# Kernel tuning notes

Hardware: AMD Instinct MI355X
Metric: run time of the kernel (lower is better)

## Reference

```python
import jax, jax.numpy as jnp
import numpy as np

N = 50000          # num nodes
E = 800000         # num edges (avg degree 16)
C_IN = 64          # input channels
TOWERS = 4
F_IN = C_IN // TOWERS       # 16 (divide_input=True)
OUT = 128
F_OUT = OUT // TOWERS       # 32
NUM_AGG = 4                 # mean, std, max, min
NUM_SC = 3                  # identity, amplification, attenuation
AVG_LOG_DEG = float(np.log(17.0))  # deg histogram: all nodes degree 16 -> log(16+1)


def setup_inputs() -> dict:
    key = jax.random.key(0)
    ks = jax.random.split(key, 10)
    nodes = jax.random.normal(ks[0], (N, C_IN), dtype=jnp.float32)
    senders = jax.random.randint(ks[1], (E,), 0, N)
    receivers = jax.random.randint(ks[2], (E,), 0, N)
    # per-tower pre-MLP: Linear(2*F_IN -> F_IN), pre_layers=1 (no activation)
    pre_w = jax.random.normal(ks[3], (TOWERS, 2 * F_IN, F_IN), dtype=jnp.float32) / np.sqrt(2 * F_IN)
    pre_b = jnp.zeros((TOWERS, F_IN), dtype=jnp.float32)
    # per-tower post-MLP: Linear(F_IN + F_IN*12 -> F_OUT), post_layers=1
    post_in = F_IN + F_IN * NUM_AGG * NUM_SC  # 208
    post_w = jax.random.normal(ks[4], (TOWERS, post_in, F_OUT), dtype=jnp.float32) / np.sqrt(post_in)
    post_b = jnp.zeros((TOWERS, F_OUT), dtype=jnp.float32)
    # final linear: TOWERS*F_OUT -> OUT
    lin_w = jax.random.normal(ks[5], (TOWERS * F_OUT, OUT), dtype=jnp.float32) / np.sqrt(TOWERS * F_OUT)
    lin_b = jnp.zeros((OUT,), dtype=jnp.float32)
    return {"nodes": nodes, "senders": senders, "receivers": receivers,
            "pre_w": pre_w, "pre_b": pre_b, "post_w": post_w, "post_b": post_b,
            "lin_w": lin_w, "lin_b": lin_b}


def reference(nodes, senders, receivers, pre_w, pre_b, post_w, post_b, lin_w, lin_b):
    # divide_input=True: split channels across towers -> [N, T, F_IN]
    x = nodes.reshape(N, TOWERS, F_IN)
    x_i = x[senders]                                  # [E, T, F_IN]
    x_j = x[receivers]                                # [E, T, F_IN]
    h = jnp.concatenate([x_i, x_j], axis=-1)          # [E, T, 2*F_IN]
    # per-tower pre-MLP (single linear), vectorized over towers
    msg = jnp.einsum('etf,tfo->eto', h, pre_w) + pre_b  # [E, T, F_IN]

    # degree-scaled multi-aggregator segment reduce over receivers
    count = jax.ops.segment_sum(jnp.ones((E,), dtype=msg.dtype), receivers, num_segments=N)  # [N]
    d = jnp.clip(count, 1.0, None)
    inv_d = (1.0 / d)[:, None, None]
    mean = jax.ops.segment_sum(msg, receivers, num_segments=N) * inv_d           # [N,T,F]
    mean_sq = jax.ops.segment_sum(msg * msg, receivers, num_segments=N) * inv_d
    std = jnp.sqrt(jax.nn.relu(mean_sq - mean * mean) + 1e-5)
    has_nb = (count > 0)[:, None, None]
    mx = jax.ops.segment_max(msg, receivers, num_segments=N)
    mx = jnp.where(has_nb, mx, 0.0)
    mn = -jax.ops.segment_max(-msg, receivers, num_segments=N)
    mn = jnp.where(has_nb, mn, 0.0)
    agg = jnp.concatenate([mean, std, mx, mn], axis=-1)  # [N, T, 4*F_IN]

    # scalers: identity, amplification, attenuation (degree clamped to >= 1)
    log_d = jnp.log(d + 1.0)[:, None, None]
    amp = log_d / AVG_LOG_DEG
    att = AVG_LOG_DEG / log_d
    scaled = jnp.concatenate([agg, agg * amp, agg * att], axis=-1)  # [N, T, 12*F_IN]

    out = jnp.concatenate([x, scaled], axis=-1)                     # [N, T, 13*F_IN]
    outs = jnp.einsum('ntf,tfo->nto', out, post_w) + post_b         # [N, T, F_OUT]
    flat = outs.reshape(N, TOWERS * F_OUT)                          # [N, 128]
    return flat @ lin_w + lin_b                                     # [N, OUT]
```

## Files before the change

### kernel.cpp

```cpp
#include <hip/hip_runtime.h>

#define AVG_LOG_DEG 2.8332133440562162f
#define CAP 64

typedef __attribute__((ext_vector_type(8))) short short8;
typedef __attribute__((ext_vector_type(4))) float f32x4;

static __device__ __forceinline__ float bl(unsigned u) { return __uint_as_float(u << 16); }
static __device__ __forceinline__ float bh(unsigned u) { return __uint_as_float(u & 0xffff0000u); }
static __device__ __forceinline__ unsigned short f2b(float f) {
    unsigned u = __float_as_uint(f);
    return (unsigned short)((u + 0x7fffu + ((u >> 16) & 1u)) >> 16);
}
static __device__ __forceinline__ unsigned pk(unsigned short lo, unsigned short hi) {
    return (unsigned)lo | ((unsigned)hi << 16);
}


__global__ void k_init(int* __restrict__ cursor, int n) {
    int i = blockIdx.x * 256 + threadIdx.x;
    if (i < n) cursor[i] = 0;
}

__global__ __launch_bounds__(256) void k_scatter2(
    const int* __restrict__ send, const int* __restrict__ recv,
    int* __restrict__ cursor, int* __restrict__ slots,
    int e, int nps)
{
    int slice = blockIdx.x & 7;
    int chunk = blockIdx.x >> 3;
    int base = chunk * 2048;
    int lo = slice * nps;
    #pragma unroll
    for (int it = 0; it < 8; ++it) {
        int i = base + it * 256 + threadIdx.x;
        if (i < e) {
            int r = recv[i];
            if ((unsigned)(r - lo) < (unsigned)nps) {
                int p = atomicAdd(&cursor[r], 1);
                if (p < CAP) slots[(size_t)r * CAP + p] = send[i];
            }
        }
    }
}


__global__ void k_prew(const float* __restrict__ post_w, const float* __restrict__ lin_w,
                       unsigned short* __restrict__ postT, unsigned short* __restrict__ linT) {
    int i = blockIdx.x * 256 + threadIdx.x;
    if (i < 28672) {
        int t = i / (32 * 224);
        int r = i % (32 * 224);
        int nn = r / 224;
        int k = r % 224;
        float wv;
        if (k < 192)      wv = post_w[((size_t)t * 208 + 16 + k) * 32 + nn];
        else if (k < 208) wv = post_w[((size_t)t * 208 + (k - 192)) * 32 + nn];
        else              wv = 0.f;
        postT[i] = f2b(wv);
    }
    int j = i - 28672;
    if (j >= 0 && j < 16384) {
        int nn = j >> 7, k = j & 127;
        linT[j] = f2b(lin_w[k * 128 + nn]);
    }
}


__global__ __launch_bounds__(256) void k_pre(
    const float* __restrict__ nodes,
    const float* __restrict__ pre_w,
    float* __restrict__ Y, int n)
{
    int lane = threadIdx.x & 63;
    int node = blockIdx.x * 4 + (threadIdx.x >> 6);
    if (node >= n) return;
    int t = lane >> 4, f = lane & 15;
    float w[16];
    #pragma unroll
    for (int k = 0; k < 16; ++k)
        w[k] = pre_w[(t * 32 + k) * 16 + f];
    const float4* xp = reinterpret_cast<const float4*>(nodes + (size_t)node * 64 + t * 16);
    float4 x0 = xp[0], x1 = xp[1], x2 = xp[2], x3 = xp[3];
    float xs[16] = {x0.x, x0.y, x0.z, x0.w, x1.x, x1.y, x1.z, x1.w,
                    x2.x, x2.y, x2.z, x2.w, x3.x, x3.y, x3.z, x3.w};
    float y = 0.f;
    #pragma unroll
    for (int k = 0; k < 16; ++k)
        y = fmaf(xs[k], w[k], y);
    Y[(size_t)node * 64 + lane] = y;
}


__global__ __launch_bounds__(256) void k_agg(
    const float* __restrict__ nodes,
    const float* __restrict__ pre_w,
    const float* __restrict__ pre_b,
    const int* __restrict__ cursor,
    const int* __restrict__ slots, const float* __restrict__ Y,
    unsigned short* __restrict__ aggh, int n)
{
    int lane = threadIdx.x & 63;
    int node = blockIdx.x * 4 + (threadIdx.x >> 6);
    if (node >= n) return;
    int t = lane >> 4, f = lane & 15;

    float w[16];
    #pragma unroll
    for (int k = 0; k < 16; ++k)
        w[k] = pre_w[(t * 32 + 16 + k) * 16 + f];
    const float4* xp = reinterpret_cast<const float4*>(nodes + (size_t)node * 64 + t * 16);
    float4 x0 = xp[0], x1 = xp[1], x2 = xp[2], x3 = xp[3];
    float xs[16] = {x0.x, x0.y, x0.z, x0.w, x1.x, x1.y, x1.z, x1.w,
                    x2.x, x2.y, x2.z, x2.w, x3.x, x3.y, x3.z, x3.w};
    float hjw = pre_b[t * 16 + f];
    #pragma unroll
    for (int k = 0; k < 16; ++k)
        hjw = fmaf(xs[k], w[k], hjw);

    int d = min(cursor[node], CAP);
    const int* sl = slots + (size_t)node * CAP;
    const float* Yp = Y + lane;
    float s = 0.f, s2 = 0.f, mx = -INFINITY, mn = INFINITY;
    int e = 0;
    for (; e + 4 <= d; e += 4) {
        int i0 = sl[e], i1 = sl[e + 1], i2 = sl[e + 2], i3 = sl[e + 3];
        float m0 = Yp[(size_t)i0 * 64] + hjw;
        float m1 = Yp[(size_t)i1 * 64] + hjw;
        float m2 = Yp[(size_t)i2 * 64] + hjw;
        float m3 = Yp[(size_t)i3 * 64] + hjw;
        s += (m0 + m1) + (m2 + m3);
        s2 = fmaf(m0, m0, s2); s2 = fmaf(m1, m1, s2);
        s2 = fmaf(m2, m2, s2); s2 = fmaf(m3, m3, s2);
        mx = fmaxf(mx, fmaxf(fmaxf(m0, m1), fmaxf(m2, m3)));
        mn = fminf(mn, fminf(fminf(m0, m1), fminf(m2, m3)));
    }
    for (; e < d; ++e) {
        int i0 = sl[e];
        float m0 = Yp[(size_t)i0 * 64] + hjw;
        s += m0;
        s2 = fmaf(m0, m0, s2);
        mx = fmaxf(mx, m0);
        mn = fminf(mn, m0);
    }

    float dc = fmaxf((float)d, 1.f);
    float inv = 1.f / dc;
    float mean = s * inv;
    float var = fmaf(-mean, mean, s2 * inv);
    float sd = sqrtf(fmaxf(var, 0.f) + 1e-5f);
    if (d == 0) { mx = 0.f; mn = 0.f; }

    unsigned short* ag = aggh + (size_t)node * 256 + t * 64 + f;
    ag[0]  = f2b(mean);
    ag[16] = f2b(sd);
    ag[32] = f2b(mx);
    ag[48] = f2b(mn);
}


__global__ __launch_bounds__(256) void k_post(
    const float* __restrict__ nodes,
    const unsigned short* __restrict__ aggh,
    const int* __restrict__ deg,
    const unsigned short* __restrict__ postT,
    const unsigned short* __restrict__ linT,
    const float* __restrict__ post_b,
    const float* __restrict__ lin_b,
    float* __restrict__ out, int n)
{
    __shared__ unsigned short sV[32 * 256];
    __shared__ unsigned short sFlat[32 * 128];
    __shared__ float sAmp[32], sAtt[32];

    int tid = threadIdx.x;
    int n0 = blockIdx.x * 32;

    if (tid < 32) {
        int g = min(n0 + tid, n - 1);
        float dc = fmaxf((float)min(deg[g], CAP), 1.f);
        float ld = logf(dc + 1.f);
        sAmp[tid] = ld * (1.f / AVG_LOG_DEG);
        sAtt[tid] = AVG_LOG_DEG / ld;
    }
    __syncthreads();

    int w = tid >> 6, lane = tid & 63;
    int quad = lane >> 4, mr = lane & 15;
    int mstrip = w & 1, nhalf = w >> 1;
    int nn = tid >> 3, j8 = tid & 7;
    int sw = nn & 7;
    int gn = min(n0 + nn, n - 1);
    int rsw = mr & 7;

    for (int t = 0; t < 4; ++t) {
        short8 bfr[7];
        {
            const unsigned short* bp = postT + (size_t)(t * 32 + nhalf * 16 + mr) * 224 + quad * 8;
            #pragma unroll
            for (int kk = 0; kk < 7; ++kk)
                bfr[kk] = *reinterpret_cast<const short8*>(bp + kk * 32);
        }

        {
            float amp = sAmp[nn], att = sAtt[nn];
            unsigned short* row = &sV[nn * 256];
            uint4 a = *reinterpret_cast<const uint4*>(aggh + (size_t)gn * 256 + t * 64 + j8 * 8);
            *reinterpret_cast<uint4*>(row + (j8 ^ sw) * 8) = a;
            unsigned uu[4] = {a.x, a.y, a.z, a.w};
            unsigned short pa[8], pb[8];
            #pragma unroll
            for (int q = 0; q < 4; ++q) {
                float lo = bl(uu[q]), hi = bh(uu[q]);
                pa[2*q]   = f2b(lo * amp); pa[2*q+1] = f2b(hi * amp);
                pb[2*q]   = f2b(lo * att); pb[2*q+1] = f2b(hi * att);
            }
            uint4 wa, wb;
            wa.x = pk(pa[0], pa[1]); wa.y = pk(pa[2], pa[3]);
            wa.z = pk(pa[4], pa[5]); wa.w = pk(pa[6], pa[7]);
            wb.x = pk(pb[0], pb[1]); wb.y = pk(pb[2], pb[3]);
            wb.z = pk(pb[4], pb[5]); wb.w = pk(pb[6], pb[7]);
            *reinterpret_cast<uint4*>(row + (8  + (j8 ^ sw)) * 8) = wa;
            *reinterpret_cast<uint4*>(row + (16 + (j8 ^ sw)) * 8) = wb;
            uint4 xw; xw.x = 0; xw.y = 0; xw.z = 0; xw.w = 0;
            if (j8 < 2) {
                const float4* xp = reinterpret_cast<const float4*>(nodes + (size_t)gn * 64 + t * 16 + j8 * 8);
                float4 xa = xp[0], xb = xp[1];
                xw.x = pk(f2b(xa.x), f2b(xa.y)); xw.y = pk(f2b(xa.z), f2b(xa.w));
                xw.z = pk(f2b(xb.x), f2b(xb.y)); xw.w = pk(f2b(xb.z), f2b(xb.w));
            }
            *reinterpret_cast<uint4*>(row + (24 + (j8 ^ sw)) * 8) = xw;
        }
        __syncthreads();

        f32x4 acc = {0.f, 0.f, 0.f, 0.f};
        const unsigned short* av0 = &sV[(mstrip * 16 + mr) * 256];
        #pragma unroll
        for (int kk = 0; kk < 7; ++kk) {
            int c = kk * 4 + quad;
            int pc = (c & ~7) | ((c & 7) ^ rsw);
            short8 avv = *reinterpret_cast<const short8*>(av0 + pc * 8);
            acc = __builtin_amdgcn_mfma_f32_16x16x32_bf16(avv, bfr[kk], acc, 0, 0, 0);
        }

        int col = t * 32 + nhalf * 16 + mr;
        float pbv = post_b[col];
        int cc = col >> 3, co = col & 7;
        #pragma unroll
        for (int i = 0; i < 4; ++i) {
            int rowf = mstrip * 16 + quad * 4 + i;
            int pc = (cc & ~7) | ((cc & 7) ^ (rowf & 7));
            sFlat[rowf * 128 + pc * 8 + co] = f2b(acc[i] + pbv);
        }
        __syncthreads();
    }

    f32x4 facc[4];
    #pragma unroll
    for (int nt = 0; nt < 4; ++nt) { facc[nt].x = 0.f; facc[nt].y = 0.f; facc[nt].z = 0.f; facc[nt].w = 0.f; }

    const unsigned short* af0 = &sFlat[(mstrip * 16 + mr) * 128];
    #pragma unroll
    for (int kk = 0; kk < 4; ++kk) {
        int c = kk * 4 + quad;
        int pc = (c & ~7) | ((c & 7) ^ rsw);
        short8 avv = *reinterpret_cast<const short8*>(af0 + pc * 8);
        #pragma unroll
        for (int nt = 0; nt < 4; ++nt) {
            short8 bv = *reinterpret_cast<const short8*>(
                linT + (size_t)(nhalf * 64 + nt * 16 + mr) * 128 + kk * 32 + quad * 8);
            facc[nt] = __builtin_amdgcn_mfma_f32_16x16x32_bf16(avv, bv, facc[nt], 0, 0, 0);
        }
    }

    #pragma unroll
    for (int nt = 0; nt < 4; ++nt) {
        int col = nhalf * 64 + nt * 16 + mr;
        float lb = lin_b[col];
        #pragma unroll
        for (int i = 0; i < 4; ++i) {
            int node = n0 + mstrip * 16 + quad * 4 + i;
            if (node < n) out[(size_t)node * 128 + col] = facc[nt][i] + lb;
        }
    }
}

extern "C" void kernel_launch(void* const* d_in, const int* in_sizes, int n_in,
                              void* d_out, int out_size, void* d_ws, size_t ws_size,
                              hipStream_t stream)
{
    const float* nodes  = (const float*)d_in[0];
    const int*   send   = (const int*)d_in[1];
    const int*   recv   = (const int*)d_in[2];
    const float* pre_w  = (const float*)d_in[3];
    const float* pre_b  = (const float*)d_in[4];
    const float* post_w = (const float*)d_in[5];
    const float* post_b = (const float*)d_in[6];
    const float* lin_w  = (const float*)d_in[7];
    const float* lin_b  = (const float*)d_in[8];
    float* out = (float*)d_out;

    int N = in_sizes[0] / 64;
    int E = in_sizes[1];
    int Npad = (N + 255) & ~255;

    int* cursor = (int*)d_ws;
    int* slots  = cursor + Npad;
    float* Y    = (float*)(slots + (size_t)Npad * CAP);
    unsigned short* aggh  = (unsigned short*)(Y + (size_t)Npad * 64);
    unsigned short* postT = aggh + (size_t)Npad * 256;
    unsigned short* linT  = postT + 28672;

    int nbN = (N + 255) / 256;
    int nps = (N + 7) / 8;
    int nbS = 8 * ((E + 2047) / 2048);

    k_prew    <<<176, 256, 0, stream>>>(post_w, lin_w, postT, linT);
    k_init    <<<nbN, 256, 0, stream>>>(cursor, N);
    k_scatter2<<<nbS, 256, 0, stream>>>(send, recv, cursor, slots, E, nps);
    k_pre     <<<(N + 3) / 4, 256, 0, stream>>>(nodes, pre_w, Y, N);
    k_agg     <<<(N + 3) / 4, 256, 0, stream>>>(nodes, pre_w, pre_b, cursor, slots, Y, aggh, N);
    k_post    <<<(N + 31) / 32, 256, 0, stream>>>(nodes, aggh, cursor, postT, linT,
                                                  post_b, lin_b, out, N);
}
```

Measured before the change: 213.7 us.

## Merge setup kernels into one launch and aggregate two nodes per wavefront

Folds the weight-transpose, cursor-init and node pre-projection kernels into one launch split by block ranges, which removes two kernel launches and the gaps between them. The aggregation kernel now gives each half-wavefront of 32 lanes one node. Each lane handles two features through float2 gathers and an 8-way unrolled neighbour loop, and writes packed bf16 pairs. This targets more memory-level parallelism and fewer issued loads per gathered row, at the cost of more registers per lane and half the lanes per node.

```diff
diff --git a/kernel.cpp b/kernel.cpp
--- a/kernel.cpp
+++ b/kernel.cpp
@@ -17,10 +17,56 @@
 }
 
 
-__global__ void k_init(int* __restrict__ cursor, int n) {
-    int i = blockIdx.x * 256 + threadIdx.x;
-    if (i < n) cursor[i] = 0;
-}
+__global__ __launch_bounds__(256) void k_setup(
+    const float* __restrict__ nodes, const float* __restrict__ pre_w,
+    const float* __restrict__ post_w, const float* __restrict__ lin_w,
+    float* __restrict__ Y, unsigned short* __restrict__ postT,
+    unsigned short* __restrict__ linT, int* __restrict__ cursor,
+    int n, int A, int nbN)
+{
+    int b = blockIdx.x;
+    if (b < A) {
+        int lane = threadIdx.x & 63;
+        int node = b * 4 + (threadIdx.x >> 6);
+        if (node >= n) return;
+        int t = lane >> 4, f = lane & 15;
+        float w[16];
+        #pragma unroll
+        for (int k = 0; k < 16; ++k)
+            w[k] = pre_w[(t * 32 + k) * 16 + f];
+        const float4* xp = reinterpret_cast<const float4*>(nodes + (size_t)node * 64 + t * 16);
+        float4 x0 = xp[0], x1 = xp[1], x2 = xp[2], x3 = xp[3];
+        float xs[16] = {x0.x, x0.y, x0.z, x0.w, x1.x, x1.y, x1.z, x1.w,
+                        x2.x, x2.y, x2.z, x2.w, x3.x, x3.y, x3.z, x3.w};
+        float y = 0.f;
+        #pragma unroll
+        for (int k = 0; k < 16; ++k)
+            y = fmaf(xs[k], w[k], y);
+        Y[(size_t)node * 64 + lane] = y;
+    } else if (b < A + 176) {
+        int i = (b - A) * 256 + threadIdx.x;
+        if (i < 28672) {
+            int t = i / (32 * 224);
+            int r = i % (32 * 224);
+            int nn = r / 224;
+            int k = r % 224;
+            float wv;
+            if (k < 192)      wv = post_w[((size_t)t * 208 + 16 + k) * 32 + nn];
+            else if (k < 208) wv = post_w[((size_t)t * 208 + (k - 192)) * 32 + nn];
+            else              wv = 0.f;
+            postT[i] = f2b(wv);
+        }
+        int j = i - 28672;
+        if (j >= 0 && j < 16384) {
+            int nn = j >> 7, k = j & 127;
+            linT[j] = f2b(lin_w[k * 128 + nn]);
+        }
+    } else {
+        int i = (b - A - 176) * 256 + threadIdx.x;
+        if (i < n) cursor[i] = 0;
+    }
+}
+
 
 __global__ __launch_bounds__(256) void k_scatter2(
     const int* __restrict__ send, const int* __restrict__ recv,
@@ -45,53 +91,6 @@
 }
 
 
-__global__ void k_prew(const float* __restrict__ post_w, const float* __restrict__ lin_w,
-                       unsigned short* __restrict__ postT, unsigned short* __restrict__ linT) {
-    int i = blockIdx.x * 256 + threadIdx.x;
-    if (i < 28672) {
-        int t = i / (32 * 224);
-        int r = i % (32 * 224);
-        int nn = r / 224;
-        int k = r % 224;
-        float wv;
-        if (k < 192)      wv = post_w[((size_t)t * 208 + 16 + k) * 32 + nn];
-        else if (k < 208) wv = post_w[((size_t)t * 208 + (k - 192)) * 32 + nn];
-        else              wv = 0.f;
-        postT[i] = f2b(wv);
-    }
-    int j = i - 28672;
-    if (j >= 0 && j < 16384) {
-        int nn = j >> 7, k = j & 127;
-        linT[j] = f2b(lin_w[k * 128 + nn]);
-    }
-}
-
-
-__global__ __launch_bounds__(256) void k_pre(
-    const float* __restrict__ nodes,
-    const float* __restrict__ pre_w,
-    float* __restrict__ Y, int n)
-{
-    int lane = threadIdx.x & 63;
-    int node = blockIdx.x * 4 + (threadIdx.x >> 6);
-    if (node >= n) return;
-    int t = lane >> 4, f = lane & 15;
-    float w[16];
-    #pragma unroll
-    for (int k = 0; k < 16; ++k)
-        w[k] = pre_w[(t * 32 + k) * 16 + f];
-    const float4* xp = reinterpret_cast<const float4*>(nodes + (size_t)node * 64 + t * 16);
-    float4 x0 = xp[0], x1 = xp[1], x2 = xp[2], x3 = xp[3];
-    float xs[16] = {x0.x, x0.y, x0.z, x0.w, x1.x, x1.y, x1.z, x1.w,
-                    x2.x, x2.y, x2.z, x2.w, x3.x, x3.y, x3.z, x3.w};
-    float y = 0.f;
-    #pragma unroll
-    for (int k = 0; k < 16; ++k)
-        y = fmaf(xs[k], w[k], y);
-    Y[(size_t)node * 64 + lane] = y;
-}
-
-
 __global__ __launch_bounds__(256) void k_agg(
     const float* __restrict__ nodes,
     const float* __restrict__ pre_w,
@@ -101,61 +100,79 @@
     unsigned short* __restrict__ aggh, int n)
 {
     int lane = threadIdx.x & 63;
-    int node = blockIdx.x * 4 + (threadIdx.x >> 6);
+    int half = lane >> 5, sub = lane & 31;
+    int node = blockIdx.x * 8 + (threadIdx.x >> 6) * 2 + half;
     if (node >= n) return;
-    int t = lane >> 4, f = lane & 15;
-
-    float w[16];
-    #pragma unroll
-    for (int k = 0; k < 16; ++k)
-        w[k] = pre_w[(t * 32 + 16 + k) * 16 + f];
-    const float4* xp = reinterpret_cast<const float4*>(nodes + (size_t)node * 64 + t * 16);
-    float4 x0 = xp[0], x1 = xp[1], x2 = xp[2], x3 = xp[3];
-    float xs[16] = {x0.x, x0.y, x0.z, x0.w, x1.x, x1.y, x1.z, x1.w,
-                    x2.x, x2.y, x2.z, x2.w, x3.x, x3.y, x3.z, x3.w};
-    float hjw = pre_b[t * 16 + f];
-    #pragma unroll
-    for (int k = 0; k < 16; ++k)
-        hjw = fmaf(xs[k], w[k], hjw);
+    int t = sub >> 3;
+    int f0 = (sub & 7) * 2;
+
+    float2 hjw;
+    {
+        const float4* xp = reinterpret_cast<const float4*>(nodes + (size_t)node * 64 + t * 16);
+        float4 x0 = xp[0], x1 = xp[1], x2 = xp[2], x3 = xp[3];
+        float xs[16] = {x0.x, x0.y, x0.z, x0.w, x1.x, x1.y, x1.z, x1.w,
+                        x2.x, x2.y, x2.z, x2.w, x3.x, x3.y, x3.z, x3.w};
+        hjw.x = pre_b[t * 16 + f0];
+        hjw.y = pre_b[t * 16 + f0 + 1];
+        #pragma unroll
+        for (int k = 0; k < 16; ++k) {
+            hjw.x = fmaf(xs[k], pre_w[(t * 32 + 16 + k) * 16 + f0],     hjw.x);
+            hjw.y = fmaf(xs[k], pre_w[(t * 32 + 16 + k) * 16 + f0 + 1], hjw.y);
+        }
+    }
 
     int d = min(cursor[node], CAP);
     const int* sl = slots + (size_t)node * CAP;
-    const float* Yp = Y + lane;
-    float s = 0.f, s2 = 0.f, mx = -INFINITY, mn = INFINITY;
+    const float* Yp = Y + sub * 2;
+
+    float2 s = {0.f, 0.f}, s2 = {0.f, 0.f};
+    float2 mx = {-INFINITY, -INFINITY}, mn = {INFINITY, INFINITY};
+
     int e = 0;
-    for (; e + 4 <= d; e += 4) {
-        int i0 = sl[e], i1 = sl[e + 1], i2 = sl[e + 2], i3 = sl[e + 3];
-        float m0 = Yp[(size_t)i0 * 64] + hjw;
-        float m1 = Yp[(size_t)i1 * 64] + hjw;
-        float m2 = Yp[(size_t)i2 * 64] + hjw;
-        float m3 = Yp[(size_t)i3 * 64] + hjw;
-        s += (m0 + m1) + (m2 + m3);
-        s2 = fmaf(m0, m0, s2); s2 = fmaf(m1, m1, s2);
-        s2 = fmaf(m2, m2, s2); s2 = fmaf(m3, m3, s2);
-        mx = fmaxf(mx, fmaxf(fmaxf(m0, m1), fmaxf(m2, m3)));
-        mn = fminf(mn, fminf(fminf(m0, m1), fminf(m2, m3)));
+    for (; e + 8 <= d; e += 8) {
+        int idx[8];
+        #pragma unroll
+        for (int q = 0; q < 8; ++q) idx[q] = sl[e + q];
+        float2 v[8];
+        #pragma unroll
+        for (int q = 0; q < 8; ++q)
+            v[q] = *reinterpret_cast<const float2*>(Yp + (size_t)idx[q] * 64);
+        #pragma unroll
+        for (int q = 0; q < 8; ++q) {
+            float2 m;
+            m.x = v[q].x + hjw.x; m.y = v[q].y + hjw.y;
+            s.x += m.x; s.y += m.y;
+            s2.x = fmaf(m.x, m.x, s2.x); s2.y = fmaf(m.y, m.y, s2.y);
+            mx.x = fmaxf(mx.x, m.x); mx.y = fmaxf(mx.y, m.y);
+            mn.x = fminf(mn.x, m.x); mn.y = fminf(mn.y, m.y);
+        }
     }
     for (; e < d; ++e) {
         int i0 = sl[e];
-        float m0 = Yp[(size_t)i0 * 64] + hjw;
-        s += m0;
-        s2 = fmaf(m0, m0, s2);
-        mx = fmaxf(mx, m0);
-        mn = fminf(mn, m0);
+        float2 v = *reinterpret_cast<const float2*>(Yp + (size_t)i0 * 64);
+        float2 m;
+        m.x = v.x + hjw.x; m.y = v.y + hjw.y;
+        s.x += m.x; s.y += m.y;
+        s2.x = fmaf(m.x, m.x, s2.x); s2.y = fmaf(m.y, m.y, s2.y);
+        mx.x = fmaxf(mx.x, m.x); mx.y = fmaxf(mx.y, m.y);
+        mn.x = fminf(mn.x, m.x); mn.y = fminf(mn.y, m.y);
     }
 
     float dc = fmaxf((float)d, 1.f);
     float inv = 1.f / dc;
-    float mean = s * inv;
-    float var = fmaf(-mean, mean, s2 * inv);
-    float sd = sqrtf(fmaxf(var, 0.f) + 1e-5f);
-    if (d == 0) { mx = 0.f; mn = 0.f; }
-
-    unsigned short* ag = aggh + (size_t)node * 256 + t * 64 + f;
-    ag[0]  = f2b(mean);
-    ag[16] = f2b(sd);
-    ag[32] = f2b(mx);
-    ag[48] = f2b(mn);
+    float2 mean, sd;
+    mean.x = s.x * inv; mean.y = s.y * inv;
+    float vx = fmaf(-mean.x, mean.x, s2.x * inv);
+    float vy = fmaf(-mean.y, mean.y, s2.y * inv);
+    sd.x = sqrtf(fmaxf(vx, 0.f) + 1e-5f);
+    sd.y = sqrtf(fmaxf(vy, 0.f) + 1e-5f);
+    if (d == 0) { mx.x = 0.f; mx.y = 0.f; mn.x = 0.f; mn.y = 0.f; }
+
+    unsigned* ag = reinterpret_cast<unsigned*>(aggh + (size_t)node * 256 + t * 64 + f0);
+    ag[0]  = pk(f2b(mean.x), f2b(mean.y));
+    ag[8]  = pk(f2b(sd.x),   f2b(sd.y));
+    ag[16] = pk(f2b(mx.x),   f2b(mx.y));
+    ag[24] = pk(f2b(mn.x),   f2b(mn.y));
 }
 
 
@@ -312,14 +329,14 @@
     unsigned short* linT  = postT + 28672;
 
     int nbN = (N + 255) / 256;
+    int A = (N + 3) / 4;
     int nps = (N + 7) / 8;
     int nbS = 8 * ((E + 2047) / 2048);
 
-    k_prew    <<<176, 256, 0, stream>>>(post_w, lin_w, postT, linT);
-    k_init    <<<nbN, 256, 0, stream>>>(cursor, N);
+    k_setup   <<<A + 176 + nbN, 256, 0, stream>>>(nodes, pre_w, post_w, lin_w,
+                                                  Y, postT, linT, cursor, N, A, nbN);
     k_scatter2<<<nbS, 256, 0, stream>>>(send, recv, cursor, slots, E, nps);
-    k_pre     <<<(N + 3) / 4, 256, 0, stream>>>(nodes, pre_w, Y, N);
-    k_agg     <<<(N + 3) / 4, 256, 0, stream>>>(nodes, pre_w, pre_b, cursor, slots, Y, aggh, N);
+    k_agg     <<<(N + 7) / 8, 256, 0, stream>>>(nodes, pre_w, pre_b, cursor, slots, Y, aggh, N);
     k_post    <<<(N + 31) / 32, 256, 0, stream>>>(nodes, aggh, cursor, postT, linT,
                                                   post_b, lin_b, out, N);
 }
```

New measurement: 212.7 us. About the same (-0.4%).
